# Optimization experiments

Measured on AMD Instinct MI355X. Metric: run time of the kernel, lower is better.

Reference implementation:

```python
import jax, jax.numpy as jnp
import numpy as np

HIDDEN = 1024
NUM_HEADS = 16
HEAD_DIM = HIDDEN // NUM_HEADS


def setup_inputs() -> dict:
    key = jax.random.key(0)
    k1, k2, k3 = jax.random.split(key, 3)
    x = jax.random.normal(k1, (2, 2048, HIDDEN), dtype=jnp.float32)
    # Linear weights, torch layout [out_features, in_features]
    w_qkv = jax.random.normal(k2, (3 * HIDDEN, HIDDEN), dtype=jnp.float32) * 0.02
    w_out = jax.random.normal(k3, (HIDDEN, HIDDEN), dtype=jnp.float32) * 0.02
    return {"x": x, "w_qkv": w_qkv, "w_out": w_out}


def reference(x, w_qkv, w_out):
    B, S, H = x.shape
    scale = 1.0 / HEAD_DIM ** 0.5
    qkv = jnp.einsum('bsh,oh->bso', x, w_qkv)              # [B,S,3H]
    qkv = qkv.reshape(B, S, 3, NUM_HEADS, HEAD_DIM)
    qkv = jnp.transpose(qkv, (2, 0, 3, 1, 4))               # [3,B,nh,S,hd]
    q, k, v = qkv[0], qkv[1], qkv[2]
    scores = jnp.einsum('bnsd,bntd->bnst', q, k) * scale    # [B,nh,S,S]
    attn = jax.nn.softmax(scores, axis=-1)
    out = jnp.einsum('bnst,bntd->bnsd', attn, v)            # [B,nh,S,hd]
    out = jnp.transpose(out, (0, 2, 1, 3)).reshape(B, S, H)
    return jnp.einsum('bsh,oh->bso', out, w_out)
```

## Files before the change

kernel.cpp:

```cpp
#include <hip/hip_runtime.h>
#include <stdint.h>

typedef unsigned short u16;
typedef __bf16 bf16x8 __attribute__((ext_vector_type(8)));
typedef float f32x4 __attribute__((ext_vector_type(4)));
typedef float f32x16 __attribute__((ext_vector_type(16)));
typedef unsigned u32x4 __attribute__((ext_vector_type(4)));

#define DEVI __device__ __forceinline__

typedef __attribute__((address_space(1))) void gvoid;
typedef __attribute__((address_space(3))) void lvoid;

DEVI u16 f2b(float f) {
  unsigned x = __builtin_bit_cast(unsigned, f);
  return (u16)((x + 0x7fffu + ((x >> 16) & 1u)) >> 16);
}

DEVI float exp2g(float x) { return __builtin_amdgcn_exp2f(x); }

DEVI void gload_lds16(const void* g, void* l) {
  __builtin_amdgcn_global_load_lds((gvoid*)g, (lvoid*)l, 16, 0, 0);
}

#define QSCALE 0.18033688011112042f

__global__ void cast_all(const float* __restrict__ x, const float* __restrict__ wqkv,
                         const float* __restrict__ wout, u16* __restrict__ outb) {
  int i = blockIdx.x * 256 + threadIdx.x;
  int stride = gridDim.x * 256;
  for (; i < 2097152; i += stride) {
    const float* src;
    float sc = 1.0f;
    if (i < 1048576) {
      src = x + 4 * (long)i;
    } else if (i < 1835008) {
      int j = i - 1048576;
      src = wqkv + 4 * (long)j;
      if (j < 262144) sc = QSCALE;
    } else {
      src = wout + 4 * (long)(i - 1835008);
    }
    float4 v = *(const float4*)src;
    ushort4 o;
    o.x = f2b(v.x * sc); o.y = f2b(v.y * sc); o.z = f2b(v.z * sc); o.w = f2b(v.w * sc);
    ((ushort4*)outb)[i] = o;
  }
}

template<int OUT, int TM, int SWZ>
__global__ __launch_bounds__(256)
void gemm_bt(const u16* __restrict__ A, const u16* __restrict__ B, void* __restrict__ Cv,
             void* __restrict__ Cv2, int M, int N, int K) {
  constexpr int MI = TM / 32;
  __shared__ u16 lA[TM * 64];
  __shared__ u16 lB[128 * 64];
  const int tid = threadIdx.x;
  const int lane = tid & 63;
  const int lr = lane & 15;
  const int lg = lane >> 4;
  const int wid = tid >> 6;

  long bm, bn;
  if (SWZ) {
    const int f = blockIdx.x + gridDim.x * blockIdx.y;
    const int chunk = (gridDim.x * gridDim.y) >> 3;
    const int ln = (f & 7) * chunk + (f >> 3);
    bm = (long)(ln % gridDim.y) * TM;
    bn = (long)(ln / gridDim.y) * 128;
  } else {
    bm = (long)blockIdx.y * TM;
    bn = (long)blockIdx.x * 128;
  }

  const int wr = (wid >> 1) * (TM / 2);
  const int wc = (wid & 1) * 64;

  f32x4 acc[MI][4];
#pragma unroll
  for (int i = 0; i < MI; ++i)
#pragma unroll
    for (int j = 0; j < 4; ++j)
      acc[i][j] = (f32x4){0.f, 0.f, 0.f, 0.f};

  for (int k0 = 0; k0 < K; k0 += 64) {
#pragma unroll
    for (int q = 0; q < MI; ++q) {
      int bi = tid + q * 256;
      int row = bi >> 3;
      int col = ((bi & 7) ^ (row & 7)) * 8;
      gload_lds16(A + (bm + row) * (long)K + k0 + col, (char*)lA + bi * 16);
    }
#pragma unroll
    for (int q = 0; q < 4; ++q) {
      int bi = tid + q * 256;
      int row = bi >> 3;
      int col = ((bi & 7) ^ (row & 7)) * 8;
      gload_lds16(B + (bn + row) * (long)K + k0 + col, (char*)lB + bi * 16);
    }
    __syncthreads();
#pragma unroll
    for (int kk = 0; kk < 2; ++kk) {
      bf16x8 af[MI], bfr[4];
      int kb = kk * 4 + lg;
#pragma unroll
      for (int mi = 0; mi < MI; ++mi) {
        int row = wr + mi * 16 + lr;
        af[mi] = *(const bf16x8*)((const char*)lA + row * 128 + ((kb ^ (row & 7)) << 4));
      }
#pragma unroll
      for (int ni = 0; ni < 4; ++ni) {
        int row = wc + ni * 16 + lr;
        bfr[ni] = *(const bf16x8*)((const char*)lB + row * 128 + ((kb ^ (row & 7)) << 4));
      }
#pragma unroll
      for (int mi = 0; mi < MI; ++mi)
#pragma unroll
        for (int ni = 0; ni < 4; ++ni)
          acc[mi][ni] = __builtin_amdgcn_mfma_f32_16x16x32_bf16(af[mi], bfr[ni], acc[mi][ni], 0, 0, 0);
    }
    __syncthreads();
  }

  if (OUT == 2 && bn >= 2048) {
#pragma unroll
    for (int mi = 0; mi < MI; ++mi)
#pragma unroll
      for (int ni = 0; ni < 4; ++ni) {
        long tok = bm + wr + mi * 16 + lg * 4;
        long ff = bn + wc + ni * 16 + lr - 2048;
        ushort4 st;
        st.x = f2b(acc[mi][ni][0]);
        st.y = f2b(acc[mi][ni][1]);
        st.z = f2b(acc[mi][ni][2]);
        st.w = f2b(acc[mi][ni][3]);
        u16* dst = (u16*)Cv2 + (((tok >> 11) << 4) + (ff >> 6)) * 131072 + (ff & 63) * 2048 + (tok & 2047);
        *(ushort4*)dst = st;
      }
  } else {
    const long strideN = (OUT == 2) ? 2048 : N;
#pragma unroll
    for (int mi = 0; mi < MI; ++mi)
#pragma unroll
      for (int ni = 0; ni < 4; ++ni)
#pragma unroll
        for (int r = 0; r < 4; ++r) {
          long row = bm + wr + mi * 16 + lg * 4 + r;
          long col = bn + wc + ni * 16 + lr;
          float v = acc[mi][ni][r];
          if (OUT == 1) ((float*)Cv)[row * strideN + col] = v;
          else          ((u16*)Cv)[row * strideN + col] = f2b(v);
        }
  }
}

__global__ __launch_bounds__(256, 2)
void attn_fwd(const u16* __restrict__ qk, const u16* __restrict__ vT,
              u16* __restrict__ outb) {
  __shared__ char SM[33280];

  const int tid = threadIdx.x;
  const int lane = tid & 63;
  const int wid = tid >> 6;
  const int ql = lane & 31;
  const int h  = lane >> 5;
  const int th = wid >> 1;
  const int qw = wid & 1;

  const int flat = blockIdx.x + (blockIdx.y << 4) + (blockIdx.z << 8);
  const int swz  = ((flat & 7) << 6) + (flat >> 3);
  const int qt = swz & 15;
  const int hd = (swz >> 4) & 15;
  const int b  = swz >> 8;

  const long rowbase = (long)b * 2048;
  const int qcol = hd * 64;
  const int kcol = 1024 + hd * 64;
  const int TSK = 64 * 2048;
  const long vhb = ((long)b * 16 + hd) * 131072;

  const int q0w = qt * 128 + qw * 64;
  bf16x8 qfA[4], qfB[4];
  {
    const u16* qpA = qk + (rowbase + q0w + ql) * 2048 + qcol + h * 8;
    const u16* qpB = qpA + 32 * 2048;
#pragma unroll
    for (int dblk = 0; dblk < 4; ++dblk) {
      qfA[dblk] = *(const bf16x8*)(qpA + dblk * 16);
      qfB[dblk] = *(const bf16x8*)(qpB + dblk * 16);
    }
  }

  float lA = 0.f, lB = 0.f;
  f32x16 oA[2], oB[2];
#pragma unroll
  for (int d = 0; d < 2; ++d)
#pragma unroll
    for (int r = 0; r < 16; ++r) { oA[d][r] = 0.f; oB[d][r] = 0.f; }

  const int c0 = tid, c1 = tid + 256;
  const int rk0 = c0 >> 3, ck0 = ((c0 & 7) ^ (rk0 & 7)) * 8;
  const int rk1 = c1 >> 3, ck1 = ((c1 & 7) ^ (rk1 & 7)) * 8;
  const int d0 = c0 * 16, d1 = c1 * 16;
  const u16* kp0 = qk + (rowbase + rk0) * 2048 + kcol + ck0;
  const u16* kp1 = qk + (rowbase + rk1) * 2048 + kcol + ck1;
  const u16* vp0 = vT + vhb + rk0 * 2048 + ck0;
  const u16* vp1 = vT + vhb + rk1 * 2048 + ck1;

  gload_lds16(kp0, SM + d0);          gload_lds16(kp1, SM + d1);
  gload_lds16(vp0, SM + 16384 + d0);  gload_lds16(vp1, SM + 16384 + d1);
  kp0 += TSK; kp1 += TSK; vp0 += 64; vp1 += 64;
  asm volatile("s_waitcnt vmcnt(0)" ::: "memory");
  __builtin_amdgcn_s_barrier();
  __builtin_amdgcn_sched_barrier(0);

  for (int tt = 0; tt < 16; ++tt) {
#pragma unroll
    for (int P = 0; P < 2; ++P) {
      char* KsCur = SM + P * 8192;
      char* VsCur = SM + 16384 + P * 8192;
      char* KsNxt = SM + (P ^ 1) * 8192;
      char* VsNxt = SM + 16384 + (P ^ 1) * 8192;

      gload_lds16(kp0, KsNxt + d0);  gload_lds16(kp1, KsNxt + d1);
      gload_lds16(vp0, VsNxt + d0);  gload_lds16(vp1, VsNxt + d1);
      kp0 += TSK; kp1 += TSK; vp0 += 64; vp1 += 64;

      f32x16 sA, sB;
#pragma unroll
      for (int r = 0; r < 16; ++r) { sA[r] = 0.f; sB[r] = 0.f; }
      const char* Kb = KsCur + (th * 32 + ql) * 128;
      __builtin_amdgcn_s_setprio(1);
#pragma unroll
      for (int kd = 0; kd < 4; ++kd) {
        bf16x8 kf = *(const bf16x8*)(Kb + (((kd * 2 + h) ^ (ql & 7)) << 4));
        sA = __builtin_amdgcn_mfma_f32_32x32x16_bf16(kf, qfA[kd], sA, 0, 0, 0);
        sB = __builtin_amdgcn_mfma_f32_32x32x16_bf16(kf, qfB[kd], sB, 0, 0, 0);
      }
      __builtin_amdgcn_s_setprio(0);

#pragma unroll
      for (int r = 0; r < 16; ++r) sA[r] = exp2g(sA[r]);
#pragma unroll
      for (int r = 0; r < 16; ++r) sB[r] = exp2g(sB[r]);
      lA += (((sA[0] + sA[1]) + (sA[2] + sA[3])) + ((sA[4] + sA[5]) + (sA[6] + sA[7])))
          + (((sA[8] + sA[9]) + (sA[10] + sA[11])) + ((sA[12] + sA[13]) + (sA[14] + sA[15])));
      lB += (((sB[0] + sB[1]) + (sB[2] + sB[3])) + ((sB[4] + sB[5]) + (sB[6] + sB[7])))
          + (((sB[8] + sB[9]) + (sB[10] + sB[11])) + ((sB[12] + sB[13]) + (sB[14] + sB[15])));

      unsigned wA[8], wB[8];
#pragma unroll
      for (int m = 0; m < 8; ++m) {
        asm("v_cvt_pk_bf16_f32 %0, %1, %2" : "=v"(wA[m]) : "v"(sA[2 * m]), "v"(sA[2 * m + 1]));
        asm("v_cvt_pk_bf16_f32 %0, %1, %2" : "=v"(wB[m]) : "v"(sB[2 * m]), "v"(sB[2 * m + 1]));
      }

      bf16x8 pbA[2], pbB[2];
#pragma unroll
      for (int ks = 0; ks < 2; ++ks) {
        unsigned a0 = wA[4 * ks],     a2 = wA[4 * ks + 2];
        unsigned a1 = wA[4 * ks + 1], a3 = wA[4 * ks + 3];
        asm("s_nop 1\n\tv_permlane32_swap_b32 %0, %1" : "+v"(a0), "+v"(a2));
        asm("s_nop 1\n\tv_permlane32_swap_b32 %0, %1" : "+v"(a1), "+v"(a3));
        u32x4 t; t[0] = a0; t[1] = a1; t[2] = a2; t[3] = a3;
        pbA[ks] = __builtin_bit_cast(bf16x8, t);
        unsigned b0 = wB[4 * ks],     b2 = wB[4 * ks + 2];
        unsigned b1 = wB[4 * ks + 1], b3 = wB[4 * ks + 3];
        asm("s_nop 1\n\tv_permlane32_swap_b32 %0, %1" : "+v"(b0), "+v"(b2));
        asm("s_nop 1\n\tv_permlane32_swap_b32 %0, %1" : "+v"(b1), "+v"(b3));
        u32x4 u; u[0] = b0; u[1] = b1; u[2] = b2; u[3] = b3;
        pbB[ks] = __builtin_bit_cast(bf16x8, u);
      }

      __builtin_amdgcn_s_setprio(1);
#pragma unroll
      for (int dblk = 0; dblk < 2; ++dblk) {
        const char* Vb = VsCur + (dblk * 32 + ql) * 128;
#pragma unroll
        for (int ks = 0; ks < 2; ++ks) {
          bf16x8 vf = *(const bf16x8*)(Vb + (((th * 4 + ks * 2 + h) ^ (ql & 7)) << 4));
          oA[dblk] = __builtin_amdgcn_mfma_f32_32x32x16_bf16(vf, pbA[ks], oA[dblk], 0, 0, 0);
          oB[dblk] = __builtin_amdgcn_mfma_f32_32x32x16_bf16(vf, pbB[ks], oB[dblk], 0, 0, 0);
        }
      }
      __builtin_amdgcn_s_setprio(0);

      asm volatile("s_waitcnt vmcnt(0)" ::: "memory");
      __builtin_amdgcn_s_barrier();
      __builtin_amdgcn_sched_barrier(0);
    }
  }
  __syncthreads();

  float pxA = lA, pyA = lA;
  asm("s_nop 1\n\tv_permlane32_swap_b32 %0, %1" : "+v"(pxA), "+v"(pyA));
  float lwA = lA + (h ? pxA : pyA);
  float pxB = lB, pyB = lB;
  asm("s_nop 1\n\tv_permlane32_swap_b32 %0, %1" : "+v"(pxB), "+v"(pyB));
  float lwB = lB + (h ? pxB : pyB);

  if (th == 1) {
    char* regA = SM + (qw * 2 + 0) * 8192;
    char* regB = SM + (qw * 2 + 1) * 8192;
#pragma unroll
    for (int dblk = 0; dblk < 2; ++dblk)
#pragma unroll
      for (int r = 0; r < 16; ++r) {
        int dl = dblk * 32 + (r & 3) + 8 * (r >> 2) + 4 * h;
        *(float*)(regA + dl * 128 + ql * 4) = oA[dblk][r];
        *(float*)(regB + dl * 128 + ql * 4) = oB[dblk][r];
      }
    if (h == 0) {
      *(float*)(SM + 32768 + (qw * 2 + 0) * 128 + ql * 4) = lwA;
      *(float*)(SM + 32768 + (qw * 2 + 1) * 128 + ql * 4) = lwB;
    }
  }
  __syncthreads();
  if (th == 0) {
    const char* regA = SM + (qw * 2 + 0) * 8192;
    const char* regB = SM + (qw * 2 + 1) * 8192;
#pragma unroll
    for (int dblk = 0; dblk < 2; ++dblk)
#pragma unroll
      for (int r = 0; r < 16; ++r) {
        int dl = dblk * 32 + (r & 3) + 8 * (r >> 2) + 4 * h;
        oA[dblk][r] += *(const float*)(regA + dl * 128 + ql * 4);
        oB[dblk][r] += *(const float*)(regB + dl * 128 + ql * 4);
      }
    float invA = 1.0f / (lwA + *(const float*)(SM + 32768 + (qw * 2 + 0) * 128 + ql * 4));
    float invB = 1.0f / (lwB + *(const float*)(SM + 32768 + (qw * 2 + 1) * 128 + ql * 4));
    long rowA = rowbase + q0w + ql;
    long rowB = rowA + 32;
#pragma unroll
    for (int dblk = 0; dblk < 2; ++dblk)
#pragma unroll
      for (int m = 0; m < 4; ++m) {
        ushort4 stA;
        stA.x = f2b(oA[dblk][4 * m + 0] * invA);
        stA.y = f2b(oA[dblk][4 * m + 1] * invA);
        stA.z = f2b(oA[dblk][4 * m + 2] * invA);
        stA.w = f2b(oA[dblk][4 * m + 3] * invA);
        *(ushort4*)(outb + rowA * 1024 + qcol + dblk * 32 + 8 * m + 4 * h) = stA;
        ushort4 stB;
        stB.x = f2b(oB[dblk][4 * m + 0] * invB);
        stB.y = f2b(oB[dblk][4 * m + 1] * invB);
        stB.z = f2b(oB[dblk][4 * m + 2] * invB);
        stB.w = f2b(oB[dblk][4 * m + 3] * invB);
        *(ushort4*)(outb + rowB * 1024 + qcol + dblk * 32 + 8 * m + 4 * h) = stB;
      }
  }
}

extern "C" void kernel_launch(void* const* d_in, const int* in_sizes, int n_in,
                              void* d_out, int out_size, void* d_ws, size_t ws_size,
                              hipStream_t stream) {
  const float* x     = (const float*)d_in[0];
  const float* w_qkv = (const float*)d_in[1];
  const float* w_out = (const float*)d_in[2];
  float* out = (float*)d_out;

  char* ws = (char*)d_ws;
  u16* xb    = (u16*)(ws);
  u16* wqkvb = (u16*)(ws + 8388608);
  u16* woutb = (u16*)(ws + 14680064);
  u16* qk    = (u16*)(ws + 16777216);
  u16* vT    = (u16*)(ws + 33554432);
  u16* attn  = (u16*)(ws + 41943040);

  cast_all<<<2048, 256, 0, stream>>>(x, w_qkv, w_out, xb);

  gemm_bt<2, 128, 1><<<dim3(24, 32), 256, 0, stream>>>(xb, wqkvb, qk, vT, 4096, 3072, 1024);

  attn_fwd<<<dim3(16, 16, 2), 256, 0, stream>>>(qk, vT, attn);

  gemm_bt<1, 64, 0><<<dim3(8, 64), 256, 0, stream>>>(attn, woutb, out, nullptr, 4096, 1024, 1024);
}
```

Baseline: 103.7 us.

## Add dedicated 256x256 double-buffered QKV GEMM kernel with async LDS loads

```diff
diff --git a/kernel.cpp b/kernel.cpp
--- a/kernel.cpp
+++ b/kernel.cpp
@@ -48,6 +48,128 @@
   }
 }
 
+__global__ __launch_bounds__(512, 2)
+void gemm_qkv(const u16* __restrict__ A, const u16* __restrict__ B,
+              u16* __restrict__ qk, u16* __restrict__ vT, int K) {
+  __shared__ u16 SA[2][256 * 64];
+  __shared__ u16 SB[2][256 * 64];
+  const int tid = threadIdx.x;
+  const int lane = tid & 63;
+  const int lr = lane & 15;
+  const int lg = lane >> 4;
+  const int wid = tid >> 6;
+  const int wm = wid >> 2;
+  const int wn = wid & 3;
+  const long bm = (long)blockIdx.y * 256;
+  const long bn = (long)blockIdx.x * 256;
+  const int wr = wm * 128;
+  const int wc = wn * 64;
+
+  f32x4 acc[8][4];
+#pragma unroll
+  for (int i = 0; i < 8; ++i)
+#pragma unroll
+    for (int j = 0; j < 4; ++j)
+      acc[i][j] = (f32x4){0.f, 0.f, 0.f, 0.f};
+
+  int srow[4], scol[4], sdst[4];
+#pragma unroll
+  for (int q = 0; q < 4; ++q) {
+    int b = tid + q * 512;
+    srow[q] = b >> 3;
+    scol[q] = ((b & 7) ^ ((b >> 3) & 7)) * 8;
+    sdst[q] = b * 16;
+  }
+
+  auto stage = [&](int buf, int k0) {
+#pragma unroll
+    for (int q = 0; q < 4; ++q)
+      gload_lds16(A + (bm + srow[q]) * (long)K + k0 + scol[q], (char*)SA[buf] + sdst[q]);
+#pragma unroll
+    for (int q = 0; q < 4; ++q)
+      gload_lds16(B + (bn + srow[q]) * (long)K + k0 + scol[q], (char*)SB[buf] + sdst[q]);
+  };
+
+  stage(0, 0);
+  asm volatile("s_waitcnt vmcnt(0)" ::: "memory");
+  __builtin_amdgcn_s_barrier();
+  __builtin_amdgcn_sched_barrier(0);
+
+  const int NITER = K >> 6;
+  for (int it = 0; it < NITER; ++it) {
+    const int cur = it & 1;
+    if (it + 1 < NITER) stage(cur ^ 1, (it + 1) * 64);
+
+    const char* cA = (const char*)SA[cur];
+    const char* cB = (const char*)SB[cur];
+
+    bf16x8 bf[4][2];
+#pragma unroll
+    for (int ni = 0; ni < 4; ++ni)
+#pragma unroll
+      for (int kk = 0; kk < 2; ++kk) {
+        int row = wc + ni * 16 + lr;
+        bf[ni][kk] = *(const bf16x8*)(cB + row * 128 + (((kk * 4 + lg) ^ (row & 7)) << 4));
+      }
+
+#pragma unroll
+    for (int half = 0; half < 2; ++half) {
+      bf16x8 af[4][2];
+#pragma unroll
+      for (int mi = 0; mi < 4; ++mi)
+#pragma unroll
+        for (int kk = 0; kk < 2; ++kk) {
+          int row = wr + half * 64 + mi * 16 + lr;
+          af[mi][kk] = *(const bf16x8*)(cA + row * 128 + (((kk * 4 + lg) ^ (row & 7)) << 4));
+        }
+      __builtin_amdgcn_s_setprio(1);
+#pragma unroll
+      for (int mi = 0; mi < 4; ++mi)
+#pragma unroll
+        for (int ni = 0; ni < 4; ++ni)
+#pragma unroll
+          for (int kk = 0; kk < 2; ++kk)
+            acc[half * 4 + mi][ni] =
+                __builtin_amdgcn_mfma_f32_16x16x32_bf16(af[mi][kk], bf[ni][kk], acc[half * 4 + mi][ni], 0, 0, 0);
+      __builtin_amdgcn_s_setprio(0);
+    }
+
+    if (it + 1 < NITER) {
+      asm volatile("s_waitcnt vmcnt(0)" ::: "memory");
+      __builtin_amdgcn_s_barrier();
+      __builtin_amdgcn_sched_barrier(0);
+    }
+  }
+
+  if (bn >= 2048) {
+#pragma unroll
+    for (int mi = 0; mi < 8; ++mi)
+#pragma unroll
+      for (int ni = 0; ni < 4; ++ni) {
+        long tok = bm + wr + mi * 16 + lg * 4;
+        long f = bn + wc + ni * 16 + lr - 2048;
+        ushort4 st;
+        st.x = f2b(acc[mi][ni][0]);
+        st.y = f2b(acc[mi][ni][1]);
+        st.z = f2b(acc[mi][ni][2]);
+        st.w = f2b(acc[mi][ni][3]);
+        u16* dst = vT + (((tok >> 11) << 4) + (f >> 6)) * 131072 + (f & 63) * 2048 + (tok & 2047);
+        *(ushort4*)dst = st;
+      }
+  } else {
+#pragma unroll
+    for (int mi = 0; mi < 8; ++mi)
+#pragma unroll
+      for (int ni = 0; ni < 4; ++ni)
+#pragma unroll
+        for (int r = 0; r < 4; ++r) {
+          long row = bm + wr + mi * 16 + lg * 4 + r;
+          long col = bn + wc + ni * 16 + lr;
+          qk[row * 2048 + col] = f2b(acc[mi][ni][r]);
+        }
+  }
+}
+
 template<int OUT, int TM, int SWZ>
 __global__ __launch_bounds__(256)
 void gemm_bt(const u16* __restrict__ A, const u16* __restrict__ B, void* __restrict__ Cv,
@@ -122,36 +244,19 @@
     __syncthreads();
   }
 
-  if (OUT == 2 && bn >= 2048) {
-#pragma unroll
-    for (int mi = 0; mi < MI; ++mi)
-#pragma unroll
-      for (int ni = 0; ni < 4; ++ni) {
-        long tok = bm + wr + mi * 16 + lg * 4;
-        long ff = bn + wc + ni * 16 + lr - 2048;
-        ushort4 st;
-        st.x = f2b(acc[mi][ni][0]);
-        st.y = f2b(acc[mi][ni][1]);
-        st.z = f2b(acc[mi][ni][2]);
-        st.w = f2b(acc[mi][ni][3]);
-        u16* dst = (u16*)Cv2 + (((tok >> 11) << 4) + (ff >> 6)) * 131072 + (ff & 63) * 2048 + (tok & 2047);
-        *(ushort4*)dst = st;
-      }
-  } else {
-    const long strideN = (OUT == 2) ? 2048 : N;
-#pragma unroll
-    for (int mi = 0; mi < MI; ++mi)
-#pragma unroll
-      for (int ni = 0; ni < 4; ++ni)
-#pragma unroll
-        for (int r = 0; r < 4; ++r) {
-          long row = bm + wr + mi * 16 + lg * 4 + r;
-          long col = bn + wc + ni * 16 + lr;
-          float v = acc[mi][ni][r];
-          if (OUT == 1) ((float*)Cv)[row * strideN + col] = v;
-          else          ((u16*)Cv)[row * strideN + col] = f2b(v);
-        }
-  }
+  const long strideN = (OUT == 2) ? 2048 : N;
+#pragma unroll
+  for (int mi = 0; mi < MI; ++mi)
+#pragma unroll
+    for (int ni = 0; ni < 4; ++ni)
+#pragma unroll
+      for (int r = 0; r < 4; ++r) {
+        long row = bm + wr + mi * 16 + lg * 4 + r;
+        long col = bn + wc + ni * 16 + lr;
+        float v = acc[mi][ni][r];
+        if (OUT == 1) ((float*)Cv)[row * strideN + col] = v;
+        else          ((u16*)Cv)[row * strideN + col] = f2b(v);
+      }
 }
 
 __global__ __launch_bounds__(256, 2)
@@ -369,7 +474,7 @@
 
   cast_all<<<2048, 256, 0, stream>>>(x, w_qkv, w_out, xb);
 
-  gemm_bt<2, 128, 1><<<dim3(24, 32), 256, 0, stream>>>(xb, wqkvb, qk, vT, 4096, 3072, 1024);
+  gemm_qkv<<<dim3(12, 16), 512, 0, stream>>>(xb, wqkvb, qk, vT, 1024);
 
   attn_fwd<<<dim3(16, 16, 2), 256, 0, stream>>>(qk, vT, attn);
 
```

Result: slower. 111.4 us (+7.4%).
